# Optimization experiments

Measured on AMD Instinct MI355X. Metric: run time of the kernel, lower is better.

## Reference

```python
import jax, jax.numpy as jnp
import numpy as np

B, IN_CH, OUT_CH, STYLE_DIM, K, H, W = 16, 512, 512, 512, 3, 32, 32


def setup_inputs() -> dict:
    key = jax.random.key(0)
    k1, k2, k3, k4 = jax.random.split(key, 4)
    return {
        "x": jax.random.normal(k1, (B, IN_CH, H, W), dtype=jnp.float32),
        "style": jax.random.normal(k2, (B, STYLE_DIM), dtype=jnp.float32),
        "aff_weight": jax.random.normal(k3, (IN_CH, STYLE_DIM), dtype=jnp.float32),
        "aff_bias": jnp.zeros((IN_CH,), dtype=jnp.float32),
        "conv_weight": jax.random.normal(k4, (OUT_CH, IN_CH, K, K), dtype=jnp.float32),
    }


def reference(x, style, aff_weight, aff_bias, conv_weight):
    # EqualizedLinearAct with act='linear': y = style @ (W*scale)^T + bias
    style_dim = aff_weight.shape[1]
    aff_scale = 1.0 / np.sqrt(style_dim)  # gain=1.0
    s = style @ (aff_weight * aff_scale).T + aff_bias + 1.0  # [B, in]

    out_ch, in_ch, k, _ = conv_weight.shape
    w_scale = 1.0 / np.sqrt(in_ch * k * k)  # gain / sqrt(in*k*k)
    # per-sample modulated weights: [B, out, in, k, k]
    w = conv_weight[None, :, :, :, :] * s[:, None, :, None, None] * w_scale
    # demodulation
    d = jax.lax.rsqrt(jnp.sum(w * w, axis=(2, 3, 4), keepdims=True) + 1e-8)
    w = w * d

    # groups=B grouped conv == per-sample conv; up=1, flip_weight=True ->
    # plain cross-correlation (same as torch F.conv2d / lax conv default).
    def conv1(xi, wi):
        # xi: [in, H, W], wi: [out, in, k, k]
        return jax.lax.conv_general_dilated(
            xi[None], wi, window_strides=(1, 1), padding="SAME",
            dimension_numbers=("NCHW", "OIHW", "NCHW"))[0]

    return jax.vmap(conv1)(x, w)  # [B, out, H, W]
```

## Files before the change

kernel.cpp:

```cpp
#include <hip/hip_runtime.h>


#define BATCH   16
#define CIN     512
#define COUT    512
#define IMG     32
#define PAD_IMG 34

static constexpr float AFF_SCALE = 0.044194173824159216f;
static constexpr float W_SCALE   = 0.014731391274719739f;

typedef __bf16 bf16x8 __attribute__((ext_vector_type(8)));
typedef float  f32x4  __attribute__((ext_vector_type(4)));

__device__ inline unsigned short f2bf(float f) {
    union { float f; unsigned int u; } v; v.f = f;
    unsigned int u = v.u;
    unsigned int r = (u + 0x7FFFu + ((u >> 16) & 1u)) >> 16;
    return (unsigned short)r;
}

__device__ inline float waveReduceSum(float v) {
    #pragma unroll
    for (int off = 32; off > 0; off >>= 1) v += __shfl_xor(v, off, 64);
    return v;
}

__global__ void prep1(const float* __restrict__ cw,
                      const float* __restrict__ style,
                      const float* __restrict__ aw,
                      const float* __restrict__ ab,
                      unsigned short* __restrict__ w_t,
                      float* __restrict__ wsq,
                      float* __restrict__ s_out) {
    const int tid = threadIdx.x;
    if (blockIdx.x < 512) {
        __shared__ float wl[4608];
        const float* src = cw + (size_t)blockIdx.x * 4608;
        for (int j = tid; j < 1152; j += 256)
            *(float4*)(wl + j * 4) = *(const float4*)(src + j * 4);
        __syncthreads();
        const int idx0 = blockIdx.x * 512 + tid * 2;
        const int base = tid * 18;
        float acc0 = 0.f, acc1 = 0.f;
        #pragma unroll
        for (int e = 0; e < 9; ++e) {
            float v0 = wl[base + e];
            float v1 = wl[base + 9 + e];
            acc0 += v0 * v0;
            acc1 += v1 * v1;
            unsigned int pk = (unsigned)f2bf(v0) | ((unsigned)f2bf(v1) << 16);
            *(unsigned int*)(w_t + (size_t)e * (COUT * CIN) + idx0) = pk;
        }
        *(float2*)(wsq + idx0) = make_float2(acc0, acc1);
    } else {
        const int q = blockIdx.x - 512;
        const int b = q >> 7;
        const int i = (q & 127) * 4 + (tid >> 6);
        const int lane = tid & 63;
        const float4* a4 = (const float4*)(aw + (size_t)i * 512);
        const float4* s4 = (const float4*)(style + (size_t)b * 512);
        float sum = 0.f;
        #pragma unroll
        for (int r = 0; r < 2; ++r) {
            float4 av = a4[lane * 2 + r];
            float4 sv = s4[lane * 2 + r];
            sum += av.x * sv.x + av.y * sv.y + av.z * sv.z + av.w * sv.w;
        }
        sum = waveReduceSum(sum);
        if (lane == 0)
            s_out[b * 512 + i] = sum * AFF_SCALE + ab[i] + 1.0f;
    }
}

__global__ void prep2(const float* __restrict__ x,
                      const float* __restrict__ s_in,
                      const float* __restrict__ wsq,
                      unsigned short* __restrict__ xpad,
                      float* __restrict__ scl) {
    const int tid = threadIdx.x;
    if (blockIdx.x >= 4352) {
        const int q = blockIdx.x - 4352;
        const int b = q >> 7;
        const int o = (q & 127) * 4 + (tid >> 6);
        const int lane = tid & 63;
        const float4* w4p = (const float4*)(wsq + (size_t)o * 512);
        const float4* s4p = (const float4*)(s_in + (size_t)b * 512);
        float sum = 0.f;
        #pragma unroll
        for (int r = 0; r < 2; ++r) {
            float4 wv = w4p[lane * 2 + r];
            float4 sv = s4p[lane * 2 + r];
            sum += sv.x * sv.x * wv.x + sv.y * sv.y * wv.y
                 + sv.z * sv.z * wv.z + sv.w * sv.w * wv.w;
        }
        sum = waveReduceSum(sum);
        if (lane == 0)
            scl[b * 512 + o] = W_SCALE * rsqrtf(W_SCALE * W_SCALE * sum + 1e-8f);
        return;
    }
    const int c0   = blockIdx.x & 7;
    const int rest = blockIdx.x >> 3;
    const int hh   = rest % 34;
    const int b    = rest / 34;
    const int c0b  = c0 * 64;
    unsigned short* rowbase = xpad + (((size_t)b * PAD_IMG + hh) * PAD_IMG) * 512;

    if (hh == 0 || hh == PAD_IMG - 1) {
        for (int j = tid; j < 34 * 32; j += 256) {
            int ww = j >> 5, cp = (j & 31) * 2;
            *(unsigned int*)(rowbase + (size_t)ww * 512 + c0b + cp) = 0u;
        }
        return;
    }

    __shared__ float t[64][33];
    const int h = hh - 1;
    #pragma unroll
    for (int r = 0; r < 2; ++r) {
        const int f   = r * 256 + tid;
        const int chl = f >> 3;
        const int w4  = (f & 7) * 4;
        float4 xv = *(const float4*)(
            x + (((size_t)b * 512 + c0b + chl) * IMG + h) * IMG + w4);
        const float sv = s_in[b * 512 + c0b + chl];
        t[chl][w4 + 0] = xv.x * sv;
        t[chl][w4 + 1] = xv.y * sv;
        t[chl][w4 + 2] = xv.z * sv;
        t[chl][w4 + 3] = xv.w * sv;
    }
    __syncthreads();
    {
        const int p  = tid >> 3;
        const int cc = (tid & 7) * 8;
        unsigned short* dst = rowbase + (size_t)(p + 1) * 512 + c0b + cc;
        uint4 pk;
        pk.x = (unsigned)f2bf(t[cc + 0][p]) | ((unsigned)f2bf(t[cc + 1][p]) << 16);
        pk.y = (unsigned)f2bf(t[cc + 2][p]) | ((unsigned)f2bf(t[cc + 3][p]) << 16);
        pk.z = (unsigned)f2bf(t[cc + 4][p]) | ((unsigned)f2bf(t[cc + 5][p]) << 16);
        pk.w = (unsigned)f2bf(t[cc + 6][p]) | ((unsigned)f2bf(t[cc + 7][p]) << 16);
        *(uint4*)dst = pk;
    }
    if (tid < 64) {
        int ww = (tid >> 5) ? (PAD_IMG - 1) : 0;
        int cp = (tid & 31) * 2;
        *(unsigned int*)(rowbase + (size_t)ww * 512 + c0b + cp) = 0u;
    }
}


#define SYNC() do {                                                           \
    asm volatile("s_waitcnt lgkmcnt(0)" ::: "memory");                        \
    __builtin_amdgcn_s_barrier();                                             \
    __builtin_amdgcn_sched_barrier(0);                                        \
} while (0)

#define LOADSTEP(stp) do {                                                    \
    const int e_  = (stp) >> 3;                                               \
    const int kc_ = ((stp) & 7) << 6;                                         \
    const int kh_ = (e_ * 11) >> 5;                                           \
    const int kw_ = e_ - kh_ * 3;                                             \
    const unsigned short* Ab_ = wt + (size_t)e_ * (COUT * CIN)                \
                                   + (size_t)m0 * 512 + kc_;                  \
    const unsigned short* Bb_ = xpad + bImgBase                               \
                              + (size_t)((h0 + kh_) * PAD_IMG + kw_) * 512    \
                              + kc_;                                          \
    ra0 = *(const uint4*)(Ab_ + aOff0);                                       \
    ra1 = *(const uint4*)(Ab_ + aOff1);                                       \
    rb0 = *(const uint4*)(Bb_ + bOff0);                                       \
    rb1 = *(const uint4*)(Bb_ + bOff1);                                       \
    rb2 = *(const uint4*)(Bb_ + bOff2);                                       \
    rb3 = *(const uint4*)(Bb_ + bOff3);                                       \
} while (0)

#define COMMIT(Albuf, Blbuf) do {                                             \
    *(uint4*)((Albuf) + lA0) = ra0;                                           \
    *(uint4*)((Albuf) + lA1) = ra1;                                           \
    *(uint4*)((Blbuf) + lB0) = rb0;                                           \
    *(uint4*)((Blbuf) + lB1) = rb1;                                           \
    *(uint4*)((Blbuf) + lB2) = rb2;                                           \
    *(uint4*)((Blbuf) + lB3) = rb3;                                           \
} while (0)

__global__ __launch_bounds__(512, 2) void conv_mfma(
    const unsigned short* __restrict__ wt,
    const unsigned short* __restrict__ xpad,
    const float* __restrict__ scl,
    float* __restrict__ out)
{
    __shared__ __align__(16) unsigned char smem[98304];
    unsigned short* Alds0 = (unsigned short*)(smem);
    unsigned short* Alds1 = (unsigned short*)(smem + 16384);
    unsigned short* Blds0 = (unsigned short*)(smem + 32768);
    unsigned short* Blds1 = (unsigned short*)(smem + 65536);
    __shared__ float sclds[128];

    const int tid = threadIdx.x;
    const int id    = blockIdx.x;
    const int xcd   = id & 7;
    const int local = id >> 3;
    const int gp    = xcd * 8 + (local >> 2);
    const int m0  = (local & 3) * 128;
    const int b   = gp >> 2;
    const int h0  = (gp & 3) * 8;

    if (tid < 128) sclds[tid] = scl[b * 512 + m0 + tid];

    const int wid  = tid >> 6;
    const int lane = tid & 63;
    const int wm = (wid >> 1) & 1;
    const int wn = wid & 1;
    const int kg = wid >> 2;

    const f32x4 vzero = {0.f, 0.f, 0.f, 0.f};
    f32x4 acc[4][8];
    #pragma unroll
    for (int i = 0; i < 4; ++i)
        #pragma unroll
        for (int j = 0; j < 8; ++j) acc[i][j] = vzero;

    int aOff0, aOff1, lA0, lA1;
    int bOff0, bOff1, bOff2, bOff3, lB0, lB1, lB2, lB3;
    {
        int f, row, c, p;
        f = tid;              row = f >> 3; c = f & 7; p = c ^ (row & 7);
        aOff0 = row * 512 + c * 8;  lA0 = row * 64 + p * 8;
        f = 512 + tid;        row = f >> 3; c = f & 7; p = c ^ (row & 7);
        aOff1 = row * 512 + c * 8;  lA1 = row * 64 + p * 8;

        f = tid;              row = f >> 3; c = f & 7; p = c ^ (row & 7);
        bOff0 = ((row >> 5) * PAD_IMG + (row & 31)) * 512 + c * 8;
        lB0 = row * 64 + p * 8;
        f = 512 + tid;        row = f >> 3; c = f & 7; p = c ^ (row & 7);
        bOff1 = ((row >> 5) * PAD_IMG + (row & 31)) * 512 + c * 8;
        lB1 = row * 64 + p * 8;
        f = 1024 + tid;       row = f >> 3; c = f & 7; p = c ^ (row & 7);
        bOff2 = ((row >> 5) * PAD_IMG + (row & 31)) * 512 + c * 8;
        lB2 = row * 64 + p * 8;
        f = 1536 + tid;       row = f >> 3; c = f & 7; p = c ^ (row & 7);
        bOff3 = ((row >> 5) * PAD_IMG + (row & 31)) * 512 + c * 8;
        lB3 = row * 64 + p * 8;
    }

    const size_t bImgBase = (size_t)b * PAD_IMG * PAD_IMG * 512;

    uint4 ra0, ra1, rb0, rb1, rb2, rb3;

    LOADSTEP(0);

    const int rl   = lane & 15;
    const int kch  = lane >> 4;
    const int swz  = ((kg * 4 + kch) ^ (rl & 7)) * 8;
    const int arow = (wm * 64 + rl) * 64;
    const int brow = (wn * 128 + rl) * 64;

    for (int step = 0; step < 72; ++step) {
        unsigned short* Ab_lds = (step & 1) ? Alds1 : Alds0;
        unsigned short* Bb_lds = (step & 1) ? Blds1 : Blds0;
        COMMIT(Ab_lds, Bb_lds);
        const int nxt = step + 1 < 72 ? step + 1 : 71;
        LOADSTEP(nxt);
        SYNC();

        bf16x8 af[4], bfr[8];
        #pragma unroll
        for (int mi = 0; mi < 4; ++mi)
            af[mi] = *(const bf16x8*)(Ab_lds + arow + mi * (16 * 64) + swz);
        bfr[0] = *(const bf16x8*)(Bb_lds + brow + 0 * (16 * 64) + swz);
        __builtin_amdgcn_sched_group_barrier(0x100, 5, 0);
        __builtin_amdgcn_s_setprio(1);
        #pragma unroll
        for (int ni = 0; ni < 8; ++ni) {
            if (ni < 7)
                bfr[ni + 1] =
                    *(const bf16x8*)(Bb_lds + brow + (ni + 1) * (16 * 64) + swz);
            #pragma unroll
            for (int mi = 0; mi < 4; ++mi)
                acc[mi][ni] = __builtin_amdgcn_mfma_f32_16x16x32_bf16(
                    af[mi], bfr[ni], acc[mi][ni], 0, 0, 0);
            if (ni < 7)
                __builtin_amdgcn_sched_group_barrier(0x100, 1, 0);
            __builtin_amdgcn_sched_group_barrier(0x008, 4, 0);
        }
        __builtin_amdgcn_s_setprio(0);
    }

    const int colp = lane & 15;
    const int rowq = (lane >> 4) * 4;
    float* ep = (float*)smem;
    float* reg = ep + wn * 8192;
    for (int wmr = 0; wmr < 2; ++wmr) {
        __syncthreads();
        if (wm == wmr && kg == 1) {
            #pragma unroll
            for (int mi = 0; mi < 4; ++mi)
                #pragma unroll
                for (int ni = 0; ni < 8; ++ni)
                    *(f32x4*)(reg + ((mi * 8 + ni) * 64 + lane) * 4) =
                        acc[mi][ni];
        }
        __syncthreads();
        if (wm == wmr && kg == 0) {
            #pragma unroll
            for (int mi = 0; mi < 4; ++mi) {
                #pragma unroll
                for (int ni = 0; ni < 8; ++ni) {
                    const f32x4 o =
                        *(const f32x4*)(reg + ((mi * 8 + ni) * 64 + lane) * 4);
                    const int p = h0 * 32 + wn * 128 + ni * 16 + colp;
                    #pragma unroll
                    for (int r2 = 0; r2 < 4; ++r2) {
                        const int ol = wm * 64 + mi * 16 + rowq + r2;
                        out[(((size_t)b * 512 + m0 + ol) << 10) + p] =
                            (acc[mi][ni][r2] + o[r2]) * sclds[ol];
                    }
                }
            }
        }
    }
}

extern "C" void kernel_launch(void* const* d_in, const int* in_sizes, int n_in,
                              void* d_out, int out_size, void* d_ws, size_t ws_size,
                              hipStream_t stream) {
    const float* x     = (const float*)d_in[0];
    const float* style = (const float*)d_in[1];
    const float* aw    = (const float*)d_in[2];
    const float* ab    = (const float*)d_in[3];
    const float* cw    = (const float*)d_in[4];
    float* out = (float*)d_out;

    char* ws = (char*)d_ws;
    float* s_buf          = (float*)(ws);
    float* scl            = (float*)(ws + 32768);
    float* wsq            = (float*)(ws + 65536);
    unsigned short* w_t   = (unsigned short*)(ws + 1114112);
    unsigned short* x_pad = (unsigned short*)(ws + 5832704);

    prep1<<<dim3(2560), 256, 0, stream>>>(cw, style, aw, ab, w_t, wsq, s_buf);
    prep2<<<dim3(6400), 256, 0, stream>>>(x, s_buf, wsq, x_pad, scl);
    conv_mfma<<<dim3(256), 512, 0, stream>>>(w_t, x_pad, scl, out);
}
```

Before: 171.2 us.

## Deepen global prefetch to two stages and interleave LDS writes with MFMAs

The main loop now keeps two register sets of global loads in flight, so each step's tile is fetched two steps ahead instead of one. The LDS writes for the next buffer are interleaved with the MFMA sequence through sched_group_barrier pins, which removes the separate commit phase before each barrier. The loop is unrolled by two to alternate the register sets and LDS buffers. This raises VGPR pressure under launch_bounds(512,2) and relies on a carefully pinned instruction schedule.

```diff
diff --git a/kernel.cpp b/kernel.cpp
--- a/kernel.cpp
+++ b/kernel.cpp
@@ -155,7 +155,7 @@
     __builtin_amdgcn_sched_barrier(0);                                        \
 } while (0)
 
-#define LOADSTEP(stp) do {                                                    \
+#define LOADSTEP(stp, S) do {                                                 \
     const int e_  = (stp) >> 3;                                               \
     const int kc_ = ((stp) & 7) << 6;                                         \
     const int kh_ = (e_ * 11) >> 5;                                           \
@@ -165,21 +165,57 @@
     const unsigned short* Bb_ = xpad + bImgBase                               \
                               + (size_t)((h0 + kh_) * PAD_IMG + kw_) * 512    \
                               + kc_;                                          \
-    ra0 = *(const uint4*)(Ab_ + aOff0);                                       \
-    ra1 = *(const uint4*)(Ab_ + aOff1);                                       \
-    rb0 = *(const uint4*)(Bb_ + bOff0);                                       \
-    rb1 = *(const uint4*)(Bb_ + bOff1);                                       \
-    rb2 = *(const uint4*)(Bb_ + bOff2);                                       \
-    rb3 = *(const uint4*)(Bb_ + bOff3);                                       \
+    ra0##S = *(const uint4*)(Ab_ + aOff0);                                    \
+    ra1##S = *(const uint4*)(Ab_ + aOff1);                                    \
+    rb0##S = *(const uint4*)(Bb_ + bOff0);                                    \
+    rb1##S = *(const uint4*)(Bb_ + bOff1);                                    \
+    rb2##S = *(const uint4*)(Bb_ + bOff2);                                    \
+    rb3##S = *(const uint4*)(Bb_ + bOff3);                                    \
 } while (0)
 
-#define COMMIT(Albuf, Blbuf) do {                                             \
-    *(uint4*)((Albuf) + lA0) = ra0;                                           \
-    *(uint4*)((Albuf) + lA1) = ra1;                                           \
-    *(uint4*)((Blbuf) + lB0) = rb0;                                           \
-    *(uint4*)((Blbuf) + lB1) = rb1;                                           \
-    *(uint4*)((Blbuf) + lB2) = rb2;                                           \
-    *(uint4*)((Blbuf) + lB3) = rb3;                                           \
+#define MFMA4(ni, bc)                                                         \
+    acc[0][ni] = __builtin_amdgcn_mfma_f32_16x16x32_bf16(af0, bc, acc[0][ni], 0, 0, 0); \
+    acc[1][ni] = __builtin_amdgcn_mfma_f32_16x16x32_bf16(af1, bc, acc[1][ni], 0, 0, 0); \
+    acc[2][ni] = __builtin_amdgcn_mfma_f32_16x16x32_bf16(af2, bc, acc[2][ni], 0, 0, 0); \
+    acc[3][ni] = __builtin_amdgcn_mfma_f32_16x16x32_bf16(af3, bc, acc[3][ni], 0, 0, 0)
+
+#define PIN_R() __builtin_amdgcn_sched_group_barrier(0x100, 1, 0)
+#define PIN_W() __builtin_amdgcn_sched_group_barrier(0x200, 1, 0)
+#define PIN_M() __builtin_amdgcn_sched_group_barrier(0x008, 4, 0)
+#define PIN_V() __builtin_amdgcn_sched_group_barrier(0x020, 3, 0)
+
+#define PHASE(ARD, BRD, AWR, BWR, CS, LS, nxt) do {                           \
+    bf16x8 af0, af1, af2, af3, bf0, bf1, bf2, bf3, bf4, bf5, bf6, bf7;        \
+    af0 = *(const bf16x8*)((ARD) + arow + 0 * 1024 + swz);                    \
+    af1 = *(const bf16x8*)((ARD) + arow + 1 * 1024 + swz);                    \
+    af2 = *(const bf16x8*)((ARD) + arow + 2 * 1024 + swz);                    \
+    af3 = *(const bf16x8*)((ARD) + arow + 3 * 1024 + swz);                    \
+    bf0 = *(const bf16x8*)((BRD) + brow + 0 * 1024 + swz);                    \
+    __builtin_amdgcn_sched_group_barrier(0x100, 5, 0);                        \
+    LOADSTEP(nxt, LS);                                                        \
+    __builtin_amdgcn_s_setprio(1);                                            \
+    bf1 = *(const bf16x8*)((BRD) + brow + 1 * 1024 + swz);                    \
+    *(uint4*)((AWR) + lA0) = ra0##CS;                                         \
+    MFMA4(0, bf0); PIN_R(); PIN_W(); PIN_M();                                 \
+    bf2 = *(const bf16x8*)((BRD) + brow + 2 * 1024 + swz);                    \
+    *(uint4*)((AWR) + lA1) = ra1##CS;                                         \
+    MFMA4(1, bf1); PIN_R(); PIN_W(); PIN_M();                                 \
+    bf3 = *(const bf16x8*)((BRD) + brow + 3 * 1024 + swz);                    \
+    *(uint4*)((BWR) + lB0) = rb0##CS;                                         \
+    MFMA4(2, bf2); PIN_R(); PIN_W(); PIN_M(); PIN_V();                        \
+    bf4 = *(const bf16x8*)((BRD) + brow + 4 * 1024 + swz);                    \
+    *(uint4*)((BWR) + lB1) = rb1##CS;                                         \
+    MFMA4(3, bf3); PIN_R(); PIN_W(); PIN_M();                                 \
+    bf5 = *(const bf16x8*)((BRD) + brow + 5 * 1024 + swz);                    \
+    *(uint4*)((BWR) + lB2) = rb2##CS;                                         \
+    MFMA4(4, bf4); PIN_R(); PIN_W(); PIN_M(); PIN_V();                        \
+    bf6 = *(const bf16x8*)((BRD) + brow + 6 * 1024 + swz);                    \
+    *(uint4*)((BWR) + lB3) = rb3##CS;                                         \
+    MFMA4(5, bf5); PIN_R(); PIN_W(); PIN_M();                                 \
+    bf7 = *(const bf16x8*)((BRD) + brow + 7 * 1024 + swz);                    \
+    MFMA4(6, bf6); PIN_R(); PIN_M();                                          \
+    MFMA4(7, bf7); PIN_M();                                                   \
+    __builtin_amdgcn_s_setprio(0);                                            \
 } while (0)
 
 __global__ __launch_bounds__(512, 2) void conv_mfma(
@@ -244,9 +280,8 @@
 
     const size_t bImgBase = (size_t)b * PAD_IMG * PAD_IMG * 512;
 
-    uint4 ra0, ra1, rb0, rb1, rb2, rb3;
-
-    LOADSTEP(0);
+    uint4 ra0A, ra1A, rb0A, rb1A, rb2A, rb3A;
+    uint4 ra0B, ra1B, rb0B, rb1B, rb2B, rb3B;
 
     const int rl   = lane & 15;
     const int kch  = lane >> 4;
@@ -254,35 +289,24 @@
     const int arow = (wm * 64 + rl) * 64;
     const int brow = (wn * 128 + rl) * 64;
 
-    for (int step = 0; step < 72; ++step) {
-        unsigned short* Ab_lds = (step & 1) ? Alds1 : Alds0;
-        unsigned short* Bb_lds = (step & 1) ? Blds1 : Blds0;
-        COMMIT(Ab_lds, Bb_lds);
-        const int nxt = step + 1 < 72 ? step + 1 : 71;
-        LOADSTEP(nxt);
+    LOADSTEP(0, A);
+    *(uint4*)(Alds0 + lA0) = ra0A;
+    *(uint4*)(Alds0 + lA1) = ra1A;
+    *(uint4*)(Blds0 + lB0) = rb0A;
+    *(uint4*)(Blds0 + lB1) = rb1A;
+    *(uint4*)(Blds0 + lB2) = rb2A;
+    *(uint4*)(Blds0 + lB3) = rb3A;
+    LOADSTEP(1, B);
+    SYNC();
+
+    for (int t = 0; t < 36; ++t) {
+        const int s = 2 * t;
+        const int n2 = (s + 2 < 72) ? s + 2 : 71;
+        const int n3 = (s + 3 < 72) ? s + 3 : 71;
+        PHASE(Alds0, Blds0, Alds1, Blds1, B, A, n2);
         SYNC();
-
-        bf16x8 af[4], bfr[8];
-        #pragma unroll
-        for (int mi = 0; mi < 4; ++mi)
-            af[mi] = *(const bf16x8*)(Ab_lds + arow + mi * (16 * 64) + swz);
-        bfr[0] = *(const bf16x8*)(Bb_lds + brow + 0 * (16 * 64) + swz);
-        __builtin_amdgcn_sched_group_barrier(0x100, 5, 0);
-        __builtin_amdgcn_s_setprio(1);
-        #pragma unroll
-        for (int ni = 0; ni < 8; ++ni) {
-            if (ni < 7)
-                bfr[ni + 1] =
-                    *(const bf16x8*)(Bb_lds + brow + (ni + 1) * (16 * 64) + swz);
-            #pragma unroll
-            for (int mi = 0; mi < 4; ++mi)
-                acc[mi][ni] = __builtin_amdgcn_mfma_f32_16x16x32_bf16(
-                    af[mi], bfr[ni], acc[mi][ni], 0, 0, 0);
-            if (ni < 7)
-                __builtin_amdgcn_sched_group_barrier(0x100, 1, 0);
-            __builtin_amdgcn_sched_group_barrier(0x008, 4, 0);
-        }
-        __builtin_amdgcn_s_setprio(0);
+        PHASE(Alds1, Blds1, Alds0, Blds0, A, B, n3);
+        SYNC();
     }
 
     const int colp = lane & 15;
```

Result: no change. 171.0 us (-0.2%).

## Stream conv operand tiles into LDS with direct global-to-LDS loads

Applied to the files above, without the earlier changes.

Replaces the register-staged global loads plus LDS stores in the conv mainloop with global_load_lds 16-byte direct DMA into the next double buffer. The XOR swizzle moves from the LDS destination into the global source addresses, and the barrier now waits on vmcnt at the end of each step. This removes the VGPR staging and the ds_write instructions, but the full vmcnt wait each step may expose load latency that the old register prefetch hid.

```diff
diff --git a/kernel.cpp b/kernel.cpp
--- a/kernel.cpp
+++ b/kernel.cpp
@@ -24,6 +24,12 @@
     #pragma unroll
     for (int off = 32; off > 0; off >>= 1) v += __shfl_xor(v, off, 64);
     return v;
+}
+
+__device__ inline void gload16(const unsigned short* g, unsigned short* l) {
+    __builtin_amdgcn_global_load_lds(
+        (const __attribute__((address_space(1))) void*)g,
+        (__attribute__((address_space(3))) void*)l, 16, 0, 0);
 }
 
 __global__ void prep1(const float* __restrict__ cw,
@@ -150,12 +156,12 @@
 
 
 #define SYNC() do {                                                           \
-    asm volatile("s_waitcnt lgkmcnt(0)" ::: "memory");                        \
+    asm volatile("s_waitcnt vmcnt(0) lgkmcnt(0)" ::: "memory");               \
     __builtin_amdgcn_s_barrier();                                             \
     __builtin_amdgcn_sched_barrier(0);                                        \
 } while (0)
 
-#define LOADSTEP(stp) do {                                                    \
+#define DMASTEP(stp, AT, BT) do {                                             \
     const int e_  = (stp) >> 3;                                               \
     const int kc_ = ((stp) & 7) << 6;                                         \
     const int kh_ = (e_ * 11) >> 5;                                           \
@@ -165,22 +171,22 @@
     const unsigned short* Bb_ = xpad + bImgBase                               \
                               + (size_t)((h0 + kh_) * PAD_IMG + kw_) * 512    \
                               + kc_;                                          \
-    ra0 = *(const uint4*)(Ab_ + aOff0);                                       \
-    ra1 = *(const uint4*)(Ab_ + aOff1);                                       \
-    rb0 = *(const uint4*)(Bb_ + bOff0);                                       \
-    rb1 = *(const uint4*)(Bb_ + bOff1);                                       \
-    rb2 = *(const uint4*)(Bb_ + bOff2);                                       \
-    rb3 = *(const uint4*)(Bb_ + bOff3);                                       \
+    gload16(Ab_ + aD0, (AT) + aL0);                                           \
+    gload16(Ab_ + aD1, (AT) + aL1);                                           \
+    gload16(Bb_ + bD0, (BT) + bL0);                                           \
+    gload16(Bb_ + bD1, (BT) + bL1);                                           \
+    gload16(Bb_ + bD2, (BT) + bL2);                                           \
+    gload16(Bb_ + bD3, (BT) + bL3);                                           \
 } while (0)
 
-#define COMMIT(Albuf, Blbuf) do {                                             \
-    *(uint4*)((Albuf) + lA0) = ra0;                                           \
-    *(uint4*)((Albuf) + lA1) = ra1;                                           \
-    *(uint4*)((Blbuf) + lB0) = rb0;                                           \
-    *(uint4*)((Blbuf) + lB1) = rb1;                                           \
-    *(uint4*)((Blbuf) + lB2) = rb2;                                           \
-    *(uint4*)((Blbuf) + lB3) = rb3;                                           \
-} while (0)
+#define MFMA4(ni, bc)                                                         \
+    acc[0][ni] = __builtin_amdgcn_mfma_f32_16x16x32_bf16(af0, bc, acc[0][ni], 0, 0, 0); \
+    acc[1][ni] = __builtin_amdgcn_mfma_f32_16x16x32_bf16(af1, bc, acc[1][ni], 0, 0, 0); \
+    acc[2][ni] = __builtin_amdgcn_mfma_f32_16x16x32_bf16(af2, bc, acc[2][ni], 0, 0, 0); \
+    acc[3][ni] = __builtin_amdgcn_mfma_f32_16x16x32_bf16(af3, bc, acc[3][ni], 0, 0, 0)
+
+#define PIN_R() __builtin_amdgcn_sched_group_barrier(0x100, 1, 0)
+#define PIN_M() __builtin_amdgcn_sched_group_barrier(0x008, 4, 0)
 
 __global__ __launch_bounds__(512, 2) void conv_mfma(
     const unsigned short* __restrict__ wt,
@@ -219,34 +225,28 @@
         #pragma unroll
         for (int j = 0; j < 8; ++j) acc[i][j] = vzero;
 
-    int aOff0, aOff1, lA0, lA1;
-    int bOff0, bOff1, bOff2, bOff3, lB0, lB1, lB2, lB3;
+    int aD0, aD1, bD0, bD1, bD2, bD3;
+    int aL0, aL1, bL0, bL1, bL2, bL3;
     {
-        int f, row, c, p;
-        f = tid;              row = f >> 3; c = f & 7; p = c ^ (row & 7);
-        aOff0 = row * 512 + c * 8;  lA0 = row * 64 + p * 8;
-        f = 512 + tid;        row = f >> 3; c = f & 7; p = c ^ (row & 7);
-        aOff1 = row * 512 + c * 8;  lA1 = row * 64 + p * 8;
-
-        f = tid;              row = f >> 3; c = f & 7; p = c ^ (row & 7);
-        bOff0 = ((row >> 5) * PAD_IMG + (row & 31)) * 512 + c * 8;
-        lB0 = row * 64 + p * 8;
-        f = 512 + tid;        row = f >> 3; c = f & 7; p = c ^ (row & 7);
-        bOff1 = ((row >> 5) * PAD_IMG + (row & 31)) * 512 + c * 8;
-        lB1 = row * 64 + p * 8;
-        f = 1024 + tid;       row = f >> 3; c = f & 7; p = c ^ (row & 7);
-        bOff2 = ((row >> 5) * PAD_IMG + (row & 31)) * 512 + c * 8;
-        lB2 = row * 64 + p * 8;
-        f = 1536 + tid;       row = f >> 3; c = f & 7; p = c ^ (row & 7);
-        bOff3 = ((row >> 5) * PAD_IMG + (row & 31)) * 512 + c * 8;
-        lB3 = row * 64 + p * 8;
+        const int l3 = lane >> 3;
+        const int cD = ((lane & 7) ^ l3) * 8;
+        const int ra = wid * 16 + l3;
+        aD0 = ra * 512 + cD;
+        aD1 = aD0 + 8 * 512;
+        aL0 = (wid * 16) * 64;
+        aL1 = (wid * 16 + 8) * 64;
+        int rb = wid * 32 + l3;
+        bD0 = ((rb >> 5) * PAD_IMG + (rb & 31)) * 512 + cD;  rb += 8;
+        bD1 = ((rb >> 5) * PAD_IMG + (rb & 31)) * 512 + cD;  rb += 8;
+        bD2 = ((rb >> 5) * PAD_IMG + (rb & 31)) * 512 + cD;  rb += 8;
+        bD3 = ((rb >> 5) * PAD_IMG + (rb & 31)) * 512 + cD;
+        bL0 = (wid * 32 +  0) * 64;
+        bL1 = (wid * 32 +  8) * 64;
+        bL2 = (wid * 32 + 16) * 64;
+        bL3 = (wid * 32 + 24) * 64;
     }
 
     const size_t bImgBase = (size_t)b * PAD_IMG * PAD_IMG * 512;
-
-    uint4 ra0, ra1, rb0, rb1, rb2, rb3;
-
-    LOADSTEP(0);
 
     const int rl   = lane & 15;
     const int kch  = lane >> 4;
@@ -254,35 +254,44 @@
     const int arow = (wm * 64 + rl) * 64;
     const int brow = (wn * 128 + rl) * 64;
 
+    DMASTEP(0, Alds0, Blds0);
+    SYNC();
+
     for (int step = 0; step < 72; ++step) {
-        unsigned short* Ab_lds = (step & 1) ? Alds1 : Alds0;
-        unsigned short* Bb_lds = (step & 1) ? Blds1 : Blds0;
-        COMMIT(Ab_lds, Bb_lds);
+        unsigned short* Ac = (step & 1) ? Alds1 : Alds0;
+        unsigned short* Bc = (step & 1) ? Blds1 : Blds0;
+        unsigned short* An = (step & 1) ? Alds0 : Alds1;
+        unsigned short* Bn = (step & 1) ? Blds0 : Blds1;
         const int nxt = step + 1 < 72 ? step + 1 : 71;
-        LOADSTEP(nxt);
-        SYNC();
-
-        bf16x8 af[4], bfr[8];
-        #pragma unroll
-        for (int mi = 0; mi < 4; ++mi)
-            af[mi] = *(const bf16x8*)(Ab_lds + arow + mi * (16 * 64) + swz);
-        bfr[0] = *(const bf16x8*)(Bb_lds + brow + 0 * (16 * 64) + swz);
+        DMASTEP(nxt, An, Bn);
+        __builtin_amdgcn_sched_group_barrier(0x020, 6, 0);
+
+        bf16x8 af0, af1, af2, af3, bf0, bf1, bf2, bf3, bf4, bf5, bf6, bf7;
+        af0 = *(const bf16x8*)(Ac + arow + 0 * 1024 + swz);
+        af1 = *(const bf16x8*)(Ac + arow + 1 * 1024 + swz);
+        af2 = *(const bf16x8*)(Ac + arow + 2 * 1024 + swz);
+        af3 = *(const bf16x8*)(Ac + arow + 3 * 1024 + swz);
+        bf0 = *(const bf16x8*)(Bc + brow + 0 * 1024 + swz);
         __builtin_amdgcn_sched_group_barrier(0x100, 5, 0);
         __builtin_amdgcn_s_setprio(1);
-        #pragma unroll
-        for (int ni = 0; ni < 8; ++ni) {
-            if (ni < 7)
-                bfr[ni + 1] =
-                    *(const bf16x8*)(Bb_lds + brow + (ni + 1) * (16 * 64) + swz);
-            #pragma unroll
-            for (int mi = 0; mi < 4; ++mi)
-                acc[mi][ni] = __builtin_amdgcn_mfma_f32_16x16x32_bf16(
-                    af[mi], bfr[ni], acc[mi][ni], 0, 0, 0);
-            if (ni < 7)
-                __builtin_amdgcn_sched_group_barrier(0x100, 1, 0);
-            __builtin_amdgcn_sched_group_barrier(0x008, 4, 0);
-        }
+        bf1 = *(const bf16x8*)(Bc + brow + 1 * 1024 + swz);
+        MFMA4(0, bf0); PIN_R(); PIN_M();
+        bf2 = *(const bf16x8*)(Bc + brow + 2 * 1024 + swz);
+        MFMA4(1, bf1); PIN_R(); PIN_M();
+        bf3 = *(const bf16x8*)(Bc + brow + 3 * 1024 + swz);
+        MFMA4(2, bf2); PIN_R(); PIN_M();
+        bf4 = *(const bf16x8*)(Bc + brow + 4 * 1024 + swz);
+        MFMA4(3, bf3); PIN_R(); PIN_M();
+        bf5 = *(const bf16x8*)(Bc + brow + 5 * 1024 + swz);
+        MFMA4(4, bf4); PIN_R(); PIN_M();
+        bf6 = *(const bf16x8*)(Bc + brow + 6 * 1024 + swz);
+        MFMA4(5, bf5); PIN_R(); PIN_M();
+        bf7 = *(const bf16x8*)(Bc + brow + 7 * 1024 + swz);
+        MFMA4(6, bf6); PIN_R(); PIN_M();
+        MFMA4(7, bf7); PIN_M();
         __builtin_amdgcn_s_setprio(0);
+
+        SYNC();
     }
 
     const int colp = lane & 15;
```

New measurement: 185.4 us. 8.3% more time.
